# Optimization experiments

Hardware: AMD Instinct MI355X
Metric: run time of the kernel (lower is better)

Reference implementation:

```python
import jax, jax.numpy as jnp
import numpy as np

K = 3
STRIDE = 1
PADDING = 1


def unfold(x, k, stride, padding):
    # torch.nn.functional.unfold: patches ordered (C, kh, kw), positions row-major
    N, C, H, W = x.shape
    xp = jnp.pad(x, ((0, 0), (0, 0), (padding, padding), (padding, padding)))
    H_out = (H - k + 2 * padding) // stride + 1
    W_out = (W - k + 2 * padding) // stride + 1
    patches = jnp.stack(
        [xp[:, :, i:i + stride * H_out:stride, j:j + stride * W_out:stride]
         for i in range(k) for j in range(k)],
        axis=2,
    )  # (N, C, k*k, H_out, W_out)
    return patches.reshape(N, C * k * k, H_out * W_out), H_out, W_out


def setup_inputs() -> dict:
    key = jax.random.key(0)
    k1, k2 = jax.random.split(key)
    x = jax.random.normal(k1, (16, 64, 14, 14), dtype=jnp.float32)
    W = jax.random.normal(k2, (64, 64, 3, 3), dtype=jnp.float32)
    return {"x": x, "W": W}


def reference(x, W):
    F_out = W.shape[0]
    X_col, H_out, W_out = unfold(x, K, STRIDE, PADDING)  # (N, D, P)
    W_col = W.reshape(F_out, -1)                          # (F, D)
    # AdderNet: out[n,f,p] = -sum_d |W[f,d] - X[n,d,p]|
    out = -jnp.sum(jnp.abs(W_col[None, :, :, None] - X_col[:, None, :, :]), axis=2)  # (N, F, P)
    return out.reshape(x.shape[0], F_out, H_out, W_out)
```

## Files before the change

kernel.cpp:

```cpp
#include <hip/hip_runtime.h>


#define N_ 16
#define C_ 64
#define F_ 64
#define H_ 14
#define W_ 14
#define P_ 196
#define RS 17
#define CH_WORDS (16*RS)
#define NT 4

__global__ __launch_bounds__(256) void adder2d_kernel(
    const float* __restrict__ x, const float* __restrict__ w,
    float* __restrict__ out)
{
    __shared__ __align__(16) float xt[C_ * CH_WORDS];

    const int tid = threadIdx.x;
    const int fg  = blockIdx.x;
    const int n   = blockIdx.y;

    float4* xt4 = (float4*)xt;
    #pragma unroll
    for (int i = 0; i < 17; ++i)
        xt4[i * 256 + tid] = make_float4(0.f, 0.f, 0.f, 0.f);
    __syncthreads();

    const float4* xv4 = (const float4*)(x + n * (C_ * P_));
    for (int idx = tid; idx < 3136; idx += 256) {
        unsigned c = (unsigned)idx / 49u;
        unsigned q = (unsigned)idx - c * 49u;
        float4 v = xv4[c * 49u + q];
        unsigned e = q * 4u;
        float vv[4] = {v.x, v.y, v.z, v.w};
        #pragma unroll
        for (int j = 0; j < 4; ++j) {
            unsigned ee  = e + j;
            unsigned r   = ee / 14u;
            unsigned col = ee - r * 14u;
            xt[c * CH_WORDS + (r + 1) * RS + (col + 1)] = vv[j];
        }
    }
    __syncthreads();

    if (tid < P_) {
        const unsigned h  = (unsigned)tid / 14u;
        const unsigned wv = (unsigned)tid - h * 14u;
        const int fbase = fg * NT;
        const float* wp = w + fbase * (C_ * 9);

        float acc0 = 0.f, acc1 = 0.f, acc2 = 0.f, acc3 = 0.f;
        const float* xrow = xt + h * RS + wv;

        #pragma unroll 2
        for (int c = 0; c < C_; ++c) {
            const float* xc = xrow + c * CH_WORDS;
            float x0 = xc[0],      x1 = xc[1],        x2 = xc[2];
            float x3 = xc[RS],     x4 = xc[RS + 1],   x5 = xc[RS + 2];
            float x6 = xc[2*RS],   x7 = xc[2*RS + 1], x8 = xc[2*RS + 2];

            const float* w0 = wp + (0 * C_ + c) * 9;
            const float* w1 = wp + (1 * C_ + c) * 9;
            const float* w2 = wp + (2 * C_ + c) * 9;
            const float* w3 = wp + (3 * C_ + c) * 9;

            acc0 += fabsf(w0[0]-x0) + fabsf(w0[1]-x1) + fabsf(w0[2]-x2)
                  + fabsf(w0[3]-x3) + fabsf(w0[4]-x4) + fabsf(w0[5]-x5)
                  + fabsf(w0[6]-x6) + fabsf(w0[7]-x7) + fabsf(w0[8]-x8);
            acc1 += fabsf(w1[0]-x0) + fabsf(w1[1]-x1) + fabsf(w1[2]-x2)
                  + fabsf(w1[3]-x3) + fabsf(w1[4]-x4) + fabsf(w1[5]-x5)
                  + fabsf(w1[6]-x6) + fabsf(w1[7]-x7) + fabsf(w1[8]-x8);
            acc2 += fabsf(w2[0]-x0) + fabsf(w2[1]-x1) + fabsf(w2[2]-x2)
                  + fabsf(w2[3]-x3) + fabsf(w2[4]-x4) + fabsf(w2[5]-x5)
                  + fabsf(w2[6]-x6) + fabsf(w2[7]-x7) + fabsf(w2[8]-x8);
            acc3 += fabsf(w3[0]-x0) + fabsf(w3[1]-x1) + fabsf(w3[2]-x2)
                  + fabsf(w3[3]-x3) + fabsf(w3[4]-x4) + fabsf(w3[5]-x5)
                  + fabsf(w3[6]-x6) + fabsf(w3[7]-x7) + fabsf(w3[8]-x8);
        }

        float* op = out + (n * F_ + fbase) * P_ + tid;
        op[0 * P_] = -acc0;
        op[1 * P_] = -acc1;
        op[2 * P_] = -acc2;
        op[3 * P_] = -acc3;
    }
}

extern "C" void kernel_launch(void* const* d_in, const int* in_sizes, int n_in,
                              void* d_out, int out_size, void* d_ws, size_t ws_size,
                              hipStream_t stream) {
    const float* x = (const float*)d_in[0];
    const float* w = (const float*)d_in[1];
    float* out = (float*)d_out;
    dim3 grid(F_ / NT, N_);
    adder2d_kernel<<<grid, 256, 0, stream>>>(x, w, out);
}
```

Measured before the change: 84.61 us.

## Transpose shared input tile to channel-innermost layout for vectorized LDS reads

The shared-memory input tile moves from a per-channel padded 2D layout to a position-major layout with channels innermost, padded to 68 floats per position. Each thread can then fetch four channels of a tap with one 128-bit LDS read, which cuts the number of shared-memory instructions in the inner loop. The staging loop now assigns one channel per thread, so global reads are strided across channels rather than contiguous, and the inner loop keeps 36 input values live in registers.

Result: no change. 85.32 us (+0.8%).

```diff
diff --git a/kernel.cpp b/kernel.cpp
--- a/kernel.cpp
+++ b/kernel.cpp
@@ -4,18 +4,15 @@
 #define N_ 16
 #define C_ 64
 #define F_ 64
-#define H_ 14
-#define W_ 14
 #define P_ 196
-#define RS 17
-#define CH_WORDS (16*RS)
+#define CPAD 68
 #define NT 4
 
 __global__ __launch_bounds__(256) void adder2d_kernel(
     const float* __restrict__ x, const float* __restrict__ w,
     float* __restrict__ out)
 {
-    __shared__ __align__(16) float xt[C_ * CH_WORDS];
+    __shared__ __align__(16) float xt[256 * CPAD];
 
     const int tid = threadIdx.x;
     const int fg  = blockIdx.x;
@@ -27,56 +24,64 @@
         xt4[i * 256 + tid] = make_float4(0.f, 0.f, 0.f, 0.f);
     __syncthreads();
 
-    const float4* xv4 = (const float4*)(x + n * (C_ * P_));
-    for (int idx = tid; idx < 3136; idx += 256) {
-        unsigned c = (unsigned)idx / 49u;
-        unsigned q = (unsigned)idx - c * 49u;
-        float4 v = xv4[c * 49u + q];
-        unsigned e = q * 4u;
-        float vv[4] = {v.x, v.y, v.z, v.w};
+    {
+        const int c  = tid & 63;
+        const int wq = tid >> 6;
+        const float4* x4 = (const float4*)(x + (n * C_ + c) * P_);
         #pragma unroll
-        for (int j = 0; j < 4; ++j) {
-            unsigned ee  = e + j;
-            unsigned r   = ee / 14u;
-            unsigned col = ee - r * 14u;
-            xt[c * CH_WORDS + (r + 1) * RS + (col + 1)] = vv[j];
+        for (int i = 0; i < 13; ++i) {
+            const int q = wq + 4 * i;
+            if (q < 49) {
+                float4 v = x4[q];
+                float vv[4] = {v.x, v.y, v.z, v.w};
+                const int e = 4 * q;
+                #pragma unroll
+                for (int j = 0; j < 4; ++j) {
+                    const int ee  = e + j;
+                    const int r   = ee / 14;
+                    const int col = ee - r * 14;
+                    xt[((r + 1) * 16 + (col + 1)) * CPAD + c] = vv[j];
+                }
+            }
         }
     }
     __syncthreads();
 
     if (tid < P_) {
-        const unsigned h  = (unsigned)tid / 14u;
-        const unsigned wv = (unsigned)tid - h * 14u;
+        const int h  = tid / 14;
+        const int wv = tid - h * 14;
         const int fbase = fg * NT;
         const float* wp = w + fbase * (C_ * 9);
 
         float acc0 = 0.f, acc1 = 0.f, acc2 = 0.f, acc3 = 0.f;
-        const float* xrow = xt + h * RS + wv;
+        const float* base = xt + (h * 16 + wv) * CPAD;
 
         #pragma unroll 2
-        for (int c = 0; c < C_; ++c) {
-            const float* xc = xrow + c * CH_WORDS;
-            float x0 = xc[0],      x1 = xc[1],        x2 = xc[2];
-            float x3 = xc[RS],     x4 = xc[RS + 1],   x5 = xc[RS + 2];
-            float x6 = xc[2*RS],   x7 = xc[2*RS + 1], x8 = xc[2*RS + 2];
+        for (int g = 0; g < 16; ++g) {
+            float4 xv[9];
+            #pragma unroll
+            for (int kh = 0; kh < 3; ++kh)
+                #pragma unroll
+                for (int kw = 0; kw < 3; ++kw)
+                    xv[kh * 3 + kw] =
+                        *(const float4*)(base + (kh * 16 + kw) * CPAD + 4 * g);
 
-            const float* w0 = wp + (0 * C_ + c) * 9;
-            const float* w1 = wp + (1 * C_ + c) * 9;
-            const float* w2 = wp + (2 * C_ + c) * 9;
-            const float* w3 = wp + (3 * C_ + c) * 9;
-
-            acc0 += fabsf(w0[0]-x0) + fabsf(w0[1]-x1) + fabsf(w0[2]-x2)
-                  + fabsf(w0[3]-x3) + fabsf(w0[4]-x4) + fabsf(w0[5]-x5)
-                  + fabsf(w0[6]-x6) + fabsf(w0[7]-x7) + fabsf(w0[8]-x8);
-            acc1 += fabsf(w1[0]-x0) + fabsf(w1[1]-x1) + fabsf(w1[2]-x2)
-                  + fabsf(w1[3]-x3) + fabsf(w1[4]-x4) + fabsf(w1[5]-x5)
-                  + fabsf(w1[6]-x6) + fabsf(w1[7]-x7) + fabsf(w1[8]-x8);
-            acc2 += fabsf(w2[0]-x0) + fabsf(w2[1]-x1) + fabsf(w2[2]-x2)
-                  + fabsf(w2[3]-x3) + fabsf(w2[4]-x4) + fabsf(w2[5]-x5)
-                  + fabsf(w2[6]-x6) + fabsf(w2[7]-x7) + fabsf(w2[8]-x8);
-            acc3 += fabsf(w3[0]-x0) + fabsf(w3[1]-x1) + fabsf(w3[2]-x2)
-                  + fabsf(w3[3]-x3) + fabsf(w3[4]-x4) + fabsf(w3[5]-x5)
-                  + fabsf(w3[6]-x6) + fabsf(w3[7]-x7) + fabsf(w3[8]-x8);
+            #pragma unroll
+            for (int f = 0; f < 4; ++f) {
+                const float* wf = wp + f * (C_ * 9) + (4 * g) * 9;
+                float a = 0.f;
+                #pragma unroll
+                for (int kk = 0; kk < 9; ++kk) {
+                    a += fabsf(wf[0 * 9 + kk] - xv[kk].x)
+                       + fabsf(wf[1 * 9 + kk] - xv[kk].y)
+                       + fabsf(wf[2 * 9 + kk] - xv[kk].z)
+                       + fabsf(wf[3 * 9 + kk] - xv[kk].w);
+                }
+                if (f == 0) acc0 += a;
+                else if (f == 1) acc1 += a;
+                else if (f == 2) acc2 += a;
+                else acc3 += a;
+            }
         }
 
         float* op = out + (n * F_ + fbase) * P_ + tid;
```
